# Kernel optimization log

Hardware: AMD Instinct MI355X
Metric: run time of the kernel (lower is better)

Reference implementation:

```python
import jax, jax.numpy as jnp
import numpy as np

M_MARGIN = 0.25
GAMMA = 256.0
NEG_INF = jnp.float32(-1e30)


def setup_inputs() -> dict:
    key = jax.random.key(0)
    k1, k2 = jax.random.split(key)
    feature = jax.random.normal(k1, (8192, 128), dtype=jnp.float32)
    label = jax.random.randint(k2, (8192,), 0, 64, dtype=jnp.int64)
    return {"feature": feature, "label": label}


def reference(feature, label):
    # F.normalize: L2-normalize rows (eps=1e-12)
    norm = jnp.maximum(jnp.linalg.norm(feature, axis=1, keepdims=True), 1e-12)
    f = feature / norm
    sim = f @ f.T  # [N, N]
    N = sim.shape[0]

    same = label[:, None] == label[None, :]
    triu = jnp.triu(jnp.ones((N, N), dtype=bool), k=1)
    pos_mask = same & triu
    neg_mask = (~same) & triu

    sim_d = jax.lax.stop_gradient(sim)  # .detach() in original
    ap = jnp.maximum(-sim_d + 1.0 + M_MARGIN, 0.0)
    an = jnp.maximum(sim_d + M_MARGIN, 0.0)
    delta_p = 1.0 - M_MARGIN
    delta_n = M_MARGIN

    logit_p = -ap * (sim - delta_p) * GAMMA
    logit_n = an * (sim - delta_n) * GAMMA

    # boolean-gather + logsumexp == masked logsumexp (fixed shapes, jit-friendly)
    lse_p = jax.nn.logsumexp(jnp.where(pos_mask, logit_p, NEG_INF))
    lse_n = jax.nn.logsumexp(jnp.where(neg_mask, logit_n, NEG_INF))

    return jax.nn.softplus(lse_n + lse_p)
```

## Files before the change

### kernel.cpp

```cpp
#include <hip/hip_runtime.h>
#include <hip/hip_bf16.h>
#include <math.h>

#define NROW 8192
#define DIM  128
#define WT   64
#define NTW  (NROW / WT)
#define NWTILE ((NTW * (NTW + 1)) / 2)
#define NBLK  (NWTILE / 4)

typedef __bf16 bf16x8 __attribute__((ext_vector_type(8)));
typedef float  f32x4  __attribute__((ext_vector_type(4)));

#define G2     369.3299304675746f
#define QPOS   (0.9375f * G2)
#define QNEG   (-0.0625f * G2)
#define NEGBIG (-3.0e38f)
#define MSENT  (-4000.0f)

__global__ __launch_bounds__(256)
void prep_kernel(const float* __restrict__ f, __hip_bfloat16* __restrict__ fhi) {
    int row  = blockIdx.x * 4 + (threadIdx.x >> 6);
    int lane = threadIdx.x & 63;
    float2 v = ((const float2*)(f + (size_t)row * DIM))[lane];
    float ss = v.x * v.x + v.y * v.y;
    #pragma unroll
    for (int off = 32; off; off >>= 1) ss += __shfl_xor(ss, off, 64);
    float inv = 1.0f / fmaxf(sqrtf(ss), 1e-12f);
    __hip_bfloat162 hv;
    hv.x = __float2bfloat16(v.x * inv);
    hv.y = __float2bfloat16(v.y * inv);
    ((__hip_bfloat162*)(fhi + (size_t)row * DIM))[lane] = hv;
}

__global__ __launch_bounds__(256, 2)
void sim_kernel(const __hip_bfloat16* __restrict__ fhi,
                const int* __restrict__ lab,
                float4* __restrict__ waveRes) {
    const int tid  = threadIdx.x;
    const int w    = tid >> 6;
    const int lane = tid & 63;
    const int lrow = lane & 15;
    const int lk   = lane >> 4;

    const int g = blockIdx.x * 4 + w;
    int tr = (int)((257.0f - sqrtf(fmaxf(66049.0f - 8.0f * (float)g, 0.f))) * 0.5f);
    if (tr > 127) tr = 127;
    if (tr < 0) tr = 0;
    while (tr > 0 && g < tr * NTW - (tr * (tr - 1)) / 2) --tr;
    while (g >= (tr + 1) * NTW - ((tr + 1) * tr) / 2) ++tr;
    const int tc = tr + (g - (tr * NTW - (tr * (tr - 1)) / 2));

    const int rowBase = tr * WT;
    const int colBase = tc * WT;
    const bool edge = (tr == tc);

    __shared__ __align__(16) char smem[4 * 16384];
    char* Abase = smem + w * 16384;
    char* Bbase = Abase + 8192;

    const int r8  = lane >> 3;
    const int kbs = ((lane & 7) << 4) ^ (r8 << 4);

    auto STAGE = [&](int c) {
        #pragma unroll
        for (int s = 0; s < 8; ++s) {
            int row = s * 8 + r8;
            const char* ga = (const char*)fhi + (size_t)(rowBase + row) * 256
                           + c * 128 + kbs;
            __builtin_amdgcn_global_load_lds(
                (const __attribute__((address_space(1))) void*)ga,
                (__attribute__((address_space(3))) void*)(Abase + s * 1024), 16, 0, 0);
        }
        #pragma unroll
        for (int s = 0; s < 8; ++s) {
            int row = s * 8 + r8;
            const char* gb = (const char*)fhi + (size_t)(colBase + row) * 256
                           + c * 128 + kbs;
            __builtin_amdgcn_global_load_lds(
                (const __attribute__((address_space(1))) void*)gb,
                (__attribute__((address_space(3))) void*)(Bbase + s * 1024), 16, 0, 0);
        }
    };

    f32x4 acc[4][4];
    #pragma unroll
    for (int mi = 0; mi < 4; ++mi)
        #pragma unroll
        for (int ni = 0; ni < 4; ++ni) acc[mi][ni] = (f32x4){0.f, 0.f, 0.f, 0.f};

    auto COMPUTE = [&]() {
        #pragma unroll
        for (int q = 0; q < 2; ++q) {
            const int kb = q * 64 + lk * 16;
            bf16x8 bfr[4];
            #pragma unroll
            for (int ni = 0; ni < 4; ++ni) {
                int rb = ni * 16 + lrow;
                bfr[ni] = *(const bf16x8*)(Bbase + rb * 128 + (kb ^ ((rb & 7) << 4)));
            }
            #pragma unroll
            for (int mi = 0; mi < 4; ++mi) {
                int ra = mi * 16 + lrow;
                bf16x8 afr = *(const bf16x8*)(Abase + ra * 128 + (kb ^ ((ra & 7) << 4)));
                #pragma unroll
                for (int ni = 0; ni < 4; ++ni)
                    acc[mi][ni] = __builtin_amdgcn_mfma_f32_16x16x32_bf16(
                        afr, bfr[ni], acc[mi][ni], 0, 0, 0);
            }
        }
    };

    STAGE(0);
    int lbv[4];
    #pragma unroll
    for (int ni = 0; ni < 4; ++ni) lbv[ni] = lab[colBase + ni * 16 + lrow];
    int4 laR[4];
    #pragma unroll
    for (int mi = 0; mi < 4; ++mi)
        laR[mi] = *(const int4*)&lab[rowBase + mi * 16 + lk * 4];

    asm volatile("s_waitcnt vmcnt(0)" ::: "memory");
    COMPUTE();
    asm volatile("s_waitcnt lgkmcnt(0)" ::: "memory");
    STAGE(1);
    asm volatile("s_waitcnt vmcnt(0)" ::: "memory");
    COMPUTE();

    float minp = 1e30f;
    float mabs = -1.0f;

#define PASS_A(EDGEF)                                                          \
    _Pragma("unroll")                                                          \
    for (int mi = 0; mi < 4; ++mi) {                                           \
        const int la[4] = {laR[mi].x, laR[mi].y, laR[mi].z, laR[mi].w};        \
        _Pragma("unroll")                                                      \
        for (int ni = 0; ni < 4; ++ni) {                                       \
            _Pragma("unroll")                                                  \
            for (int r = 0; r < 4; ++r) {                                      \
                float s = acc[mi][ni][r];                                      \
                bool pos = (la[r] == lbv[ni]);                                 \
                float t = fmaxf(s, -0.25f);                                    \
                bool valid = true;                                             \
                if (EDGEF) {                                                   \
                    int il = mi * 16 + lk * 4 + r;                             \
                    int jl = ni * 16 + lrow;                                   \
                    valid = (jl > il);                                         \
                    pos = pos && valid;                                        \
                }                                                              \
                float u = pos ? s : t;                                         \
                minp = fminf(minp, pos ? s : 1e30f);                           \
                bool nm = EDGEF ? (valid && !pos) : !pos;                      \
                mabs = fmaxf(mabs, nm ? fabsf(t) : -1.0f);                     \
                acc[mi][ni][r] = u;                                            \
            }                                                                  \
        }                                                                      \
    }
    if (edge) { PASS_A(true) } else { PASS_A(false) }
#undef PASS_A

    #pragma unroll
    for (int off = 32; off; off >>= 1) {
        minp = fminf(minp, __shfl_xor(minp, off, 64));
        mabs = fmaxf(mabs, __shfl_xor(mabs, off, 64));
    }
    const float Mp = (minp < 2.0f)
        ? fmaf(G2, minp * minp, fmaf(-2.0f * G2, minp, QPOS)) : MSENT;
    const float Mn = (mabs >= 0.0f) ? fmaf(G2, mabs * mabs, QNEG) : MSENT;
    const float qph = QPOS - Mp;
    const float qnh = QNEG - Mn;
    float sp = 0.f, sn = 0.f;

#define PASS_B(EDGEF)                                                          \
    _Pragma("unroll")                                                          \
    for (int mi = 0; mi < 4; ++mi) {                                           \
        const int la[4] = {laR[mi].x, laR[mi].y, laR[mi].z, laR[mi].w};        \
        _Pragma("unroll")                                                      \
        for (int ni = 0; ni < 4; ++ni) {                                       \
            _Pragma("unroll")                                                  \
            for (int r = 0; r < 4; ++r) {                                      \
                float u = acc[mi][ni][r];                                      \
                bool pos = (la[r] == lbv[ni]);                                 \
                float P  = pos ? (-2.0f * G2) : 0.0f;                          \
                float Qh = pos ? qph : qnh;                                    \
                float e = __builtin_amdgcn_exp2f(                              \
                              fmaf(G2, u * u, fmaf(P, u, Qh)));                \
                if (EDGEF) {                                                   \
                    int il = mi * 16 + lk * 4 + r;                             \
                    int jl = ni * 16 + lrow;                                   \
                    e = (jl > il) ? e : 0.f;                                   \
                }                                                              \
                float ep = pos ? e : 0.f;                                      \
                sp += ep;                                                      \
                sn += (e - ep);                                                \
            }                                                                  \
        }                                                                      \
    }
    if (edge) { PASS_B(true) } else { PASS_B(false) }
#undef PASS_B

    #pragma unroll
    for (int off = 32; off; off >>= 1) {
        sp += __shfl_xor(sp, off, 64);
        sn += __shfl_xor(sn, off, 64);
    }
    if (lane == 0) waveRes[g] = make_float4(Mp, sp, Mn, sn);
}

__global__ __launch_bounds__(1024)
void final_kernel(const float4* __restrict__ waveRes, float* __restrict__ out) {
    __shared__ float red[16][4];
    const int tid  = threadIdx.x;
    const int wv   = tid >> 6;
    const int lane = tid & 63;

    float4 e[9];
    int ne = 0;
    for (int i = tid; i < NWTILE; i += 1024) e[ne++] = waveRes[i];

    float mp = NEGBIG, mn = NEGBIG;
    for (int k = 0; k < ne; ++k) {
        mp = fmaxf(mp, e[k].x);
        mn = fmaxf(mn, e[k].z);
    }
    #pragma unroll
    for (int off = 32; off; off >>= 1) {
        mp = fmaxf(mp, __shfl_xor(mp, off, 64));
        mn = fmaxf(mn, __shfl_xor(mn, off, 64));
    }
    if (lane == 0) { red[wv][0] = mp; red[wv][1] = mn; }
    __syncthreads();
    float MP = red[0][0], MN = red[0][1];
    #pragma unroll
    for (int q = 1; q < 16; ++q) {
        MP = fmaxf(MP, red[q][0]);
        MN = fmaxf(MN, red[q][1]);
    }

    float sp = 0.f, sn = 0.f;
    for (int k = 0; k < ne; ++k) {
        sp = fmaf(e[k].y, __builtin_amdgcn_exp2f(e[k].x - MP), sp);
        sn = fmaf(e[k].w, __builtin_amdgcn_exp2f(e[k].z - MN), sn);
    }
    #pragma unroll
    for (int off = 32; off; off >>= 1) {
        sp += __shfl_xor(sp, off, 64);
        sn += __shfl_xor(sn, off, 64);
    }
    __syncthreads();
    if (lane == 0) { red[wv][2] = sp; red[wv][3] = sn; }
    __syncthreads();
    if (tid == 0) {
        float Sp = 0.f, Sn = 0.f;
        #pragma unroll
        for (int q = 0; q < 16; ++q) { Sp += red[q][2]; Sn += red[q][3]; }
        const double LN2 = 0.6931471805599453;
        double lse_p = ((double)MP + log2((double)Sp)) * LN2;
        double lse_n = ((double)MN + log2((double)Sn)) * LN2;
        double xx = lse_p + lse_n;
        double r = (xx > 30.0) ? xx : log1p(exp(xx));
        out[0] = (float)r;
    }
}

extern "C" void kernel_launch(void* const* d_in, const int* in_sizes, int n_in,
                              void* d_out, int out_size, void* d_ws, size_t ws_size,
                              hipStream_t stream) {
    const float* f   = (const float*)d_in[0];
    const int*   lab = (const int*)d_in[1];
    float*  out      = (float*)d_out;

    __hip_bfloat16* fhi = (__hip_bfloat16*)d_ws;
    float4* waveRes = (float4*)((char*)d_ws + 4u * 1024 * 1024);

    prep_kernel<<<NROW / 4, 256, 0, stream>>>(f, fhi);
    sim_kernel<<<NBLK, 256, 0, stream>>>(fhi, lab, waveRes);
    final_kernel<<<1, 1024, 0, stream>>>(waveRes, out);
}
```

Baseline: 54.29 us.

## Share 128x128 block tile across four waves via common LDS staging

Replaces per-wave independent 64x64 tiles with a 128x128 block tile where four waves compute 2x2 sub-tiles from shared LDS copies of A and B rows. This halves global/L2 reads of the normalized features and stages labels in shared memory. It drops the two-stage K pipelining in favour of a single full load plus block barrier, and diagonal blocks waste a larger fraction of work.

Result: slower. 55.73 us (+2.7%).

```diff
diff --git a/kernel.cpp b/kernel.cpp
--- a/kernel.cpp
+++ b/kernel.cpp
@@ -4,10 +4,10 @@
 
 #define NROW 8192
 #define DIM  128
-#define WT   64
-#define NTW  (NROW / WT)
-#define NWTILE ((NTW * (NTW + 1)) / 2)
-#define NBLK  (NWTILE / 4)
+#define BT   128
+#define NT   (NROW / BT)
+#define NBLK ((NT * (NT + 1)) / 2)
+#define NWR  (NBLK * 4)
 
 typedef __bf16 bf16x8 __attribute__((ext_vector_type(8)));
 typedef float  f32x4  __attribute__((ext_vector_type(4)));
@@ -36,96 +36,92 @@
 __global__ __launch_bounds__(256, 2)
 void sim_kernel(const __hip_bfloat16* __restrict__ fhi,
                 const int* __restrict__ lab,
-                float4* __restrict__ waveRes) {
+                float4* __restrict__ blockRes) {
     const int tid  = threadIdx.x;
     const int w    = tid >> 6;
     const int lane = tid & 63;
     const int lrow = lane & 15;
     const int lk   = lane >> 4;
 
-    const int g = blockIdx.x * 4 + w;
-    int tr = (int)((257.0f - sqrtf(fmaxf(66049.0f - 8.0f * (float)g, 0.f))) * 0.5f);
-    if (tr > 127) tr = 127;
-    if (tr < 0) tr = 0;
-    while (tr > 0 && g < tr * NTW - (tr * (tr - 1)) / 2) --tr;
-    while (g >= (tr + 1) * NTW - ((tr + 1) * tr) / 2) ++tr;
-    const int tc = tr + (g - (tr * NTW - (tr * (tr - 1)) / 2));
-
-    const int rowBase = tr * WT;
-    const int colBase = tc * WT;
+    int bid = blockIdx.x;
+    int tr = (int)((129.0f - sqrtf(16641.0f - 8.0f * (float)bid)) * 0.5f);
+    while (tr > 0 && bid < tr * NT - (tr * (tr - 1)) / 2) --tr;
+    while (bid >= (tr + 1) * NT - ((tr + 1) * tr) / 2) ++tr;
+    const int tc = tr + (bid - (tr * NT - (tr * (tr - 1)) / 2));
+
+    const int rowBase = tr * BT;
+    const int colBase = tc * BT;
     const bool edge = (tr == tc);
 
-    __shared__ __align__(16) char smem[4 * 16384];
-    char* Abase = smem + w * 16384;
-    char* Bbase = Abase + 8192;
-
-    const int r8  = lane >> 3;
-    const int kbs = ((lane & 7) << 4) ^ (r8 << 4);
-
-    auto STAGE = [&](int c) {
-        #pragma unroll
-        for (int s = 0; s < 8; ++s) {
-            int row = s * 8 + r8;
-            const char* ga = (const char*)fhi + (size_t)(rowBase + row) * 256
-                           + c * 128 + kbs;
-            __builtin_amdgcn_global_load_lds(
-                (const __attribute__((address_space(1))) void*)ga,
-                (__attribute__((address_space(3))) void*)(Abase + s * 1024), 16, 0, 0);
+    __shared__ __align__(16) char smem[64 * 1024];
+    __shared__ int labA[BT];
+    __shared__ int labB[BT];
+    char* As = smem;
+    char* Bs = smem + 32 * 1024;
+
+    if (tid < BT)            labA[tid] = lab[rowBase + tid];
+    else if (tid < 2 * BT)   labB[tid - BT] = lab[colBase + (tid - BT)];
+
+    const int rsub4 = lane >> 4;
+    const int col16 = (lane & 15) << 4;
+
+    #pragma unroll
+    for (int t = 0; t < 16; ++t) {
+        int seg = w * 16 + t;
+        int arr = seg >> 5;
+        int s32 = seg & 31;
+        int row = s32 * 4 + rsub4;
+        const char* g = (const char*)fhi
+            + (size_t)((arr ? colBase : rowBase) + row) * 256
+            + (col16 ^ ((row & 7) << 4));
+        char* ldsb = (arr ? Bs : As) + s32 * 1024;
+        __builtin_amdgcn_global_load_lds(
+            (const __attribute__((address_space(1))) void*)g,
+            (__attribute__((address_space(3))) void*)ldsb, 16, 0, 0);
+    }
+
+    f32x4 acc[4][4];
+    #pragma unroll
+    for (int mi = 0; mi < 4; ++mi)
+        #pragma unroll
+        for (int ni = 0; ni < 4; ++ni) acc[mi][ni] = (f32x4){0.f, 0.f, 0.f, 0.f};
+
+    const int mrow0 = (w >> 1) * 64;
+    const int ncol0 = (w & 1) * 64;
+
+    __syncthreads();
+
+    #pragma unroll
+    for (int q = 0; q < 4; ++q) {
+        const int kb = q * 64 + lk * 16;
+        bf16x8 bfr[4];
+        #pragma unroll
+        for (int ni = 0; ni < 4; ++ni) {
+            int rb = colBase ? (ncol0 + ni * 16 + lrow) : (ncol0 + ni * 16 + lrow);
+            rb = ncol0 + ni * 16 + lrow;
+            bfr[ni] = *(const bf16x8*)(Bs + rb * 256 + (kb ^ ((rb & 7) << 4)));
         }
-        #pragma unroll
-        for (int s = 0; s < 8; ++s) {
-            int row = s * 8 + r8;
-            const char* gb = (const char*)fhi + (size_t)(colBase + row) * 256
-                           + c * 128 + kbs;
-            __builtin_amdgcn_global_load_lds(
-                (const __attribute__((address_space(1))) void*)gb,
-                (__attribute__((address_space(3))) void*)(Bbase + s * 1024), 16, 0, 0);
+        bf16x8 afr[4];
+        #pragma unroll
+        for (int mi = 0; mi < 4; ++mi) {
+            int ra = mrow0 + mi * 16 + lrow;
+            afr[mi] = *(const bf16x8*)(As + ra * 256 + (kb ^ ((ra & 7) << 4)));
         }
-    };
-
-    f32x4 acc[4][4];
+        #pragma unroll
+        for (int mi = 0; mi < 4; ++mi)
+            #pragma unroll
+            for (int ni = 0; ni < 4; ++ni)
+                acc[mi][ni] = __builtin_amdgcn_mfma_f32_16x16x32_bf16(
+                    afr[mi], bfr[ni], acc[mi][ni], 0, 0, 0);
+    }
+
+    int lbv[4];
+    #pragma unroll
+    for (int ni = 0; ni < 4; ++ni) lbv[ni] = labB[ncol0 + ni * 16 + lrow];
+    int4 laR[4];
     #pragma unroll
     for (int mi = 0; mi < 4; ++mi)
-        #pragma unroll
-        for (int ni = 0; ni < 4; ++ni) acc[mi][ni] = (f32x4){0.f, 0.f, 0.f, 0.f};
-
-    auto COMPUTE = [&]() {
-        #pragma unroll
-        for (int q = 0; q < 2; ++q) {
-            const int kb = q * 64 + lk * 16;
-            bf16x8 bfr[4];
-            #pragma unroll
-            for (int ni = 0; ni < 4; ++ni) {
-                int rb = ni * 16 + lrow;
-                bfr[ni] = *(const bf16x8*)(Bbase + rb * 128 + (kb ^ ((rb & 7) << 4)));
-            }
-            #pragma unroll
-            for (int mi = 0; mi < 4; ++mi) {
-                int ra = mi * 16 + lrow;
-                bf16x8 afr = *(const bf16x8*)(Abase + ra * 128 + (kb ^ ((ra & 7) << 4)));
-                #pragma unroll
-                for (int ni = 0; ni < 4; ++ni)
-                    acc[mi][ni] = __builtin_amdgcn_mfma_f32_16x16x32_bf16(
-                        afr, bfr[ni], acc[mi][ni], 0, 0, 0);
-            }
-        }
-    };
-
-    STAGE(0);
-    int lbv[4];
-    #pragma unroll
-    for (int ni = 0; ni < 4; ++ni) lbv[ni] = lab[colBase + ni * 16 + lrow];
-    int4 laR[4];
-    #pragma unroll
-    for (int mi = 0; mi < 4; ++mi)
-        laR[mi] = *(const int4*)&lab[rowBase + mi * 16 + lk * 4];
-
-    asm volatile("s_waitcnt vmcnt(0)" ::: "memory");
-    COMPUTE();
-    asm volatile("s_waitcnt lgkmcnt(0)" ::: "memory");
-    STAGE(1);
-    asm volatile("s_waitcnt vmcnt(0)" ::: "memory");
-    COMPUTE();
+        laR[mi] = *(const int4*)&labA[mrow0 + mi * 16 + lk * 4];
 
     float minp = 1e30f;
     float mabs = -1.0f;
@@ -143,8 +139,8 @@
                 float t = fmaxf(s, -0.25f);                                    \
                 bool valid = true;                                             \
                 if (EDGEF) {                                                   \
-                    int il = mi * 16 + lk * 4 + r;                             \
-                    int jl = ni * 16 + lrow;                                   \
+                    int il = mrow0 + mi * 16 + lk * 4 + r;                     \
+                    int jl = ncol0 + ni * 16 + lrow;                           \
                     valid = (jl > il);                                         \
                     pos = pos && valid;                                        \
                 }                                                              \
@@ -186,8 +182,8 @@
                 float e = __builtin_amdgcn_exp2f(                              \
                               fmaf(G2, u * u, fmaf(P, u, Qh)));                \
                 if (EDGEF) {                                                   \
-                    int il = mi * 16 + lk * 4 + r;                             \
-                    int jl = ni * 16 + lrow;                                   \
+                    int il = mrow0 + mi * 16 + lk * 4 + r;                     \
+                    int jl = ncol0 + ni * 16 + lrow;                           \
                     e = (jl > il) ? e : 0.f;                                   \
                 }                                                              \
                 float ep = pos ? e : 0.f;                                      \
@@ -204,7 +200,7 @@
         sp += __shfl_xor(sp, off, 64);
         sn += __shfl_xor(sn, off, 64);
     }
-    if (lane == 0) waveRes[g] = make_float4(Mp, sp, Mn, sn);
+    if (lane == 0) blockRes[bid * 4 + w] = make_float4(Mp, sp, Mn, sn);
 }
 
 __global__ __launch_bounds__(1024)
@@ -216,7 +212,7 @@
 
     float4 e[9];
     int ne = 0;
-    for (int i = tid; i < NWTILE; i += 1024) e[ne++] = waveRes[i];
+    for (int i = tid; i < NWR; i += 1024) e[ne++] = waveRes[i];
 
     float mp = NEGBIG, mn = NEGBIG;
     for (int k = 0; k < ne; ++k) {
@@ -271,9 +267,9 @@
     float*  out      = (float*)d_out;
 
     __hip_bfloat16* fhi = (__hip_bfloat16*)d_ws;
-    float4* waveRes = (float4*)((char*)d_ws + 4u * 1024 * 1024);
+    float4* blockRes = (float4*)((char*)d_ws + 4u * 1024 * 1024);
 
     prep_kernel<<<NROW / 4, 256, 0, stream>>>(f, fhi);
-    sim_kernel<<<NBLK, 256, 0, stream>>>(fhi, lab, waveRes);
-    final_kernel<<<1, 1024, 0, stream>>>(waveRes, out);
-}
+    sim_kernel<<<NBLK, 256, 0, stream>>>(fhi, lab, blockRes);
+    final_kernel<<<1, 1024, 0, stream>>>(blockRes, out);
+}
```
